# Kernel tuning notes

Hardware: AMD Instinct MI355X
Metric: run time of the kernel (lower is better)

The kernel has to match this reference:

```python
import jax, jax.numpy as jnp
import numpy as np

N_HEADS = 4

def log_cosh(x):
    # numerically stable log(cosh(x)) = |x| + log1p(exp(-2|x|)) - log(2)
    ax = jnp.abs(x)
    return ax + jnp.log1p(jnp.exp(-2.0 * ax)) - jnp.log(2.0)

def setup_inputs() -> dict:
    key = jax.random.key(0)
    ks = jax.random.split(key, 7)
    B, I, A, E, H = 4, 2048, 2048, 256, N_HEADS
    return {
        "query": jax.random.normal(ks[0], (B, I, E), dtype=jnp.float32),
        "key": jax.random.normal(ks[1], (B, A, E), dtype=jnp.float32),
        "value": jax.random.normal(ks[2], (B, A, E), dtype=jnp.float32),
        "distances": jax.random.uniform(ks[3], (B, I, A), dtype=jnp.float32),
        "in_proj_w": jax.random.normal(ks[4], (3 * E, E), dtype=jnp.float32) * 0.05,
        "out_proj_w": jax.random.normal(ks[5], (E, E), dtype=jnp.float32) * 0.05,
        "mass_w": jax.random.normal(ks[6], (H, E), dtype=jnp.float32) * 0.05,
    }

def reference(query, key, value, distances, in_proj_w, out_proj_w, mass_w):
    B, I, E = query.shape
    A = key.shape[1]
    H = N_HEADS
    D = E // H
    # distance-decay additive bias: mass is (B, A, H), nonnegative via log_cosh
    mass = log_cosh(key @ mass_w.T)                       # (B, A, H)
    bias = jnp.einsum('bah,bia->bhia', -mass, distances)  # (B, H, I, A)
    # nn.MultiheadAttention (bias=False) projections
    wq, wk, wv = jnp.split(in_proj_w, 3, axis=0)          # each (E, E)
    q = (query @ wq.T).reshape(B, I, H, D).transpose(0, 2, 1, 3)  # (B,H,I,D)
    k = (key @ wk.T).reshape(B, A, H, D).transpose(0, 2, 1, 3)    # (B,H,A,D)
    v = (value @ wv.T).reshape(B, A, H, D).transpose(0, 2, 1, 3)  # (B,H,A,D)
    scale = 1.0 / jnp.sqrt(jnp.asarray(D, dtype=q.dtype))
    scores = jnp.einsum('bhid,bhad->bhia', q, k) * scale + bias
    attn = jax.nn.softmax(scores, axis=-1)
    o = jnp.einsum('bhia,bhad->bhid', attn, v)            # (B,H,I,D)
    o = o.transpose(0, 2, 1, 3).reshape(B, I, E)
    return o @ out_proj_w.T
```

## Files before the change

### kernel.cpp

```cpp
#include <hip/hip_runtime.h>
#include <hip/hip_bf16.h>
#include <math.h>

#define BB 4
#define II 2048
#define AA 2048
#define EE 256
#define HH 4

#define LOG2E 1.4426950408889634f
#define SCL   (0.125f * LOG2E)

typedef __bf16 bf16_t;
typedef bf16_t bf16x8 __attribute__((ext_vector_type(8)));
typedef bf16_t bf16x4 __attribute__((ext_vector_type(4)));
typedef float  f32x4  __attribute__((ext_vector_type(4)));

static __device__ __forceinline__ f32x4 mfma16(bf16x8 a, bf16x8 b, f32x4 c) {
    return __builtin_amdgcn_mfma_f32_16x16x32_bf16(a, b, c, 0, 0, 0);
}

static __device__ __forceinline__ void glds16(const bf16_t* g, const bf16_t* l) {
    __builtin_amdgcn_global_load_lds(
        (const __attribute__((address_space(1))) void*)g,
        (__attribute__((address_space(3))) void*)l, 16, 0, 0);
}

static __device__ __forceinline__ void proj_body(
    const float* __restrict__ Aop, const float* __restrict__ Bop,
    bf16_t* __restrict__ Cout, int m0, int n0, int TRANS, float cscale,
    bf16_t (*sA)[72], bf16_t (*sB)[72])
{
    const int t = threadIdx.x;
    const int w = t >> 6, l = t & 63, g = l >> 4, q = l & 15;
    const int wm = w >> 1, wn = w & 1;
    const int r = t >> 2, s = t & 3;

    f32x4 acc[2][2] = {};

    for (int kt = 0; kt < 4; ++kt) {
        {
            const float* ga = Aop + (size_t)(m0 + r) * EE + kt * 64 + s * 16;
            float tmp[16];
            *(f32x4*)&tmp[0]  = *(const f32x4*)(ga + 0);
            *(f32x4*)&tmp[4]  = *(const f32x4*)(ga + 4);
            *(f32x4*)&tmp[8]  = *(const f32x4*)(ga + 8);
            *(f32x4*)&tmp[12] = *(const f32x4*)(ga + 12);
            bf16x8 w0, w1;
            #pragma unroll
            for (int i = 0; i < 8; ++i) { w0[i] = (bf16_t)tmp[i]; w1[i] = (bf16_t)tmp[8 + i]; }
            *(bf16x8*)&sA[r][s * 16]     = w0;
            *(bf16x8*)&sA[r][s * 16 + 8] = w1;
        }
        {
            const float* gb = Bop + (size_t)(n0 + r) * EE + kt * 64 + s * 16;
            float tmp[16];
            *(f32x4*)&tmp[0]  = *(const f32x4*)(gb + 0);
            *(f32x4*)&tmp[4]  = *(const f32x4*)(gb + 4);
            *(f32x4*)&tmp[8]  = *(const f32x4*)(gb + 8);
            *(f32x4*)&tmp[12] = *(const f32x4*)(gb + 12);
            bf16x8 w0, w1;
            #pragma unroll
            for (int i = 0; i < 8; ++i) { w0[i] = (bf16_t)tmp[i]; w1[i] = (bf16_t)tmp[8 + i]; }
            *(bf16x8*)&sB[r][s * 16]     = w0;
            *(bf16x8*)&sB[r][s * 16 + 8] = w1;
        }
        __syncthreads();
        #pragma unroll
        for (int ks = 0; ks < 2; ++ks) {
            bf16x8 aA[2], aB[2];
            #pragma unroll
            for (int f = 0; f < 2; ++f) {
                aA[f] = *(const bf16x8*)&sA[wm * 32 + f * 16 + q][ks * 32 + g * 8];
                aB[f] = *(const bf16x8*)&sB[wn * 32 + f * 16 + q][ks * 32 + g * 8];
            }
            #pragma unroll
            for (int fm = 0; fm < 2; ++fm)
            #pragma unroll
            for (int fn = 0; fn < 2; ++fn)
                acc[fm][fn] = mfma16(aA[fm], aB[fn], acc[fm][fn]);
        }
        __syncthreads();
    }
    #pragma unroll
    for (int fm = 0; fm < 2; ++fm)
    #pragma unroll
    for (int fn = 0; fn < 2; ++fn)
    #pragma unroll
    for (int j = 0; j < 4; ++j) {
        const int m = m0 + wm * 32 + fm * 16 + g * 4 + j;
        const int n = n0 + wn * 32 + fn * 16 + q;
        const bf16_t v = (bf16_t)(acc[fm][fn][j] * cscale);
        if (TRANS == 0) {
            Cout[(size_t)m * EE + n] = v;
        } else {
            const int bb = n >> 11, a = n & (AA - 1);
            const int a6 = a & 63;
            const int p6 = (a6 & 32) | ((a6 & 12) << 1) | ((a6 & 16) >> 2) | (a6 & 3);
            Cout[(size_t)bb * (AA * EE) + (size_t)(a >> 6) * (EE * 64) + m * 64 + p6] = v;
        }
    }
}

__global__ __launch_bounds__(256) void fused_pre(
    const float* __restrict__ query, const float* __restrict__ key,
    const float* __restrict__ value, const float* __restrict__ in_w,
    const float* __restrict__ mass_w,
    bf16_t* __restrict__ Qp, bf16_t* __restrict__ Kp, bf16_t* __restrict__ Vt,
    float* __restrict__ massT)
{
    __shared__ __align__(16) bf16_t sA[64][72];
    __shared__ __align__(16) bf16_t sB[64][72];
    const int z = blockIdx.z;
    if (z == 0) {
        proj_body(query, in_w, Qp, blockIdx.x * 64, blockIdx.y * 64, 0, SCL, sA, sB);
    } else if (z == 1) {
        proj_body(key, in_w + 65536, Kp, blockIdx.x * 64, blockIdx.y * 64, 0, 1.0f, sA, sB);
    } else if (z == 2) {
        proj_body(in_w + 131072, value, Vt, blockIdx.y * 64, blockIdx.x * 64, 1, 1.0f, sA, sB);
    } else {
        const int w = threadIdx.x >> 6, l = threadIdx.x & 63;
        const int p = blockIdx.y * 128 + blockIdx.x;
        const int row0 = p * 16 + w * 4;
        f32x4 mw[HH];
        #pragma unroll
        for (int hh = 0; hh < HH; ++hh)
            mw[hh] = *(const f32x4*)(mass_w + hh * EE + l * 4);
        #pragma unroll
        for (int rr = 0; rr < 4; ++rr) {
            const int row = row0 + rr;
            f32x4 kv = *(const f32x4*)(key + (size_t)row * EE + l * 4);
            f32x4 sd;
            #pragma unroll
            for (int hh = 0; hh < HH; ++hh)
                sd[hh] = kv[0]*mw[hh][0] + kv[1]*mw[hh][1] + kv[2]*mw[hh][2] + kv[3]*mw[hh][3];
            #pragma unroll
            for (int off = 32; off >= 1; off >>= 1) {
                #pragma unroll
                for (int hh = 0; hh < HH; ++hh) sd[hh] += __shfl_xor(sd[hh], off, 64);
            }
            if (l == 0) {
                const int bb = row >> 11, a = row & (AA - 1);
                #pragma unroll
                for (int hh = 0; hh < HH; ++hh) {
                    float ax = fabsf(sd[hh]);
                    massT[((size_t)bb * HH + hh) * AA + a] =
                        (ax + log1pf(__expf(-2.0f * ax)) - 0.693147180559945f) * LOG2E;
                }
            }
        }
    }
}

__global__ __launch_bounds__(256) void out_gemm(
    const bf16_t* __restrict__ Aop, const float* __restrict__ Bop,
    float* __restrict__ Cout)
{
    __shared__ __align__(16) bf16_t sA[64][72];
    __shared__ __align__(16) bf16_t sB[64][72];
    const int t = threadIdx.x;
    const int w = t >> 6, l = t & 63, g = l >> 4, q = l & 15;
    const int wm = w >> 1, wn = w & 1;
    const int m0 = blockIdx.x * 64, n0 = blockIdx.y * 64;
    const int r = t >> 2, s = t & 3;

    f32x4 acc[2][2] = {};

    for (int kt = 0; kt < 4; ++kt) {
        {
            const bf16_t* ga = Aop + (size_t)(m0 + r) * EE + kt * 64 + s * 16;
            *(bf16x8*)&sA[r][s * 16]     = *(const bf16x8*)(ga);
            *(bf16x8*)&sA[r][s * 16 + 8] = *(const bf16x8*)(ga + 8);
        }
        {
            const float* gb = Bop + (size_t)(n0 + r) * EE + kt * 64 + s * 16;
            float tmp[16];
            *(f32x4*)&tmp[0]  = *(const f32x4*)(gb + 0);
            *(f32x4*)&tmp[4]  = *(const f32x4*)(gb + 4);
            *(f32x4*)&tmp[8]  = *(const f32x4*)(gb + 8);
            *(f32x4*)&tmp[12] = *(const f32x4*)(gb + 12);
            bf16x8 w0, w1;
            #pragma unroll
            for (int i = 0; i < 8; ++i) { w0[i] = (bf16_t)tmp[i]; w1[i] = (bf16_t)tmp[8 + i]; }
            *(bf16x8*)&sB[r][s * 16]     = w0;
            *(bf16x8*)&sB[r][s * 16 + 8] = w1;
        }
        __syncthreads();
        #pragma unroll
        for (int ks = 0; ks < 2; ++ks) {
            bf16x8 aA[2], aB[2];
            #pragma unroll
            for (int f = 0; f < 2; ++f) {
                aA[f] = *(const bf16x8*)&sA[wm * 32 + f * 16 + q][ks * 32 + g * 8];
                aB[f] = *(const bf16x8*)&sB[wn * 32 + f * 16 + q][ks * 32 + g * 8];
            }
            #pragma unroll
            for (int fm = 0; fm < 2; ++fm)
            #pragma unroll
            for (int fn = 0; fn < 2; ++fn)
                acc[fm][fn] = mfma16(aA[fm], aB[fn], acc[fm][fn]);
        }
        __syncthreads();
    }
    #pragma unroll
    for (int fm = 0; fm < 2; ++fm)
    #pragma unroll
    for (int fn = 0; fn < 2; ++fn)
    #pragma unroll
    for (int j = 0; j < 4; ++j) {
        const int m = m0 + wm * 32 + fm * 16 + g * 4 + j;
        const int n = n0 + wn * 32 + fn * 16 + q;
        Cout[(size_t)m * EE + n] = acc[fm][fn][j];
    }
}

__global__ __launch_bounds__(256, 4) void attn_kernel(
    const bf16_t* __restrict__ Qp, const bf16_t* __restrict__ Kp,
    const bf16_t* __restrict__ Vt, const float* __restrict__ massT,
    const float* __restrict__ dist, bf16_t* __restrict__ Obuf)
{
    __shared__ __align__(16) bf16_t sK[2][4096];
    __shared__ __align__(16) bf16_t sV[2][4096];
    __shared__ __align__(16) float  sM[2048];

    const int t = threadIdx.x;
    const int rg = t >> 6, l = t & 63, g = l >> 4, q = l & 15;
    const int h = blockIdx.y, b = blockIdx.z;
    const int i0 = blockIdx.x * 64;

    *(f32x4*)&sM[t * 8]     = *(const f32x4*)(massT + ((size_t)b * HH + h) * AA + t * 8);
    *(f32x4*)&sM[t * 8 + 4] = *(const f32x4*)(massT + ((size_t)b * HH + h) * AA + t * 8 + 4);

    bf16x8 qf[2];
    #pragma unroll
    for (int ks = 0; ks < 2; ++ks)
        qf[ks] = *(const bf16x8*)(Qp + (size_t)(b * II + i0 + rg * 16 + q) * EE
                                     + h * 64 + ks * 32 + g * 8);

    const int u0 = rg * 2;
    const int drow0 = u0 * 8 + (l >> 3);
    const int cs = (l & 7) ^ (drow0 & 7);

    const bf16_t* pkg = Kp + ((size_t)b * AA + drow0) * EE + h * 64 + cs * 8;
    const bf16_t* pvg = Vt + (size_t)b * (AA * EE) + (size_t)(h * 64 + drow0) * 64 + cs * 8;
    const float*  pdg = dist + ((size_t)b * II + i0 + rg * 16 + q) * AA + g * 4;

    auto stage = [&](int kb) {
        #pragma unroll
        for (int u = 0; u < 2; ++u) {
            glds16(pkg + u * (8 * EE), &sK[kb][(u0 + u) * 512]);
            glds16(pvg + u * (8 * 64), &sV[kb][(u0 + u) * 512]);
        }
    };

    f32x4 rd[2][4];

    stage(0);
    pkg += 64 * EE; pvg += EE * 64;
    #pragma unroll
    for (int fa = 0; fa < 4; ++fa) rd[0][fa] = *(const f32x4*)(pdg + fa * 16);
    pdg += 64;
    __syncthreads();

    float mrun = -INFINITY;
    f32x4 oacc[4] = {};
    f32x4 lacc = {};
    bf16x8 vone;
    #pragma unroll
    for (int j = 0; j < 8; ++j) vone[j] = (bf16_t)1.0f;

    int ma = 0;

    #pragma unroll 2
    for (int k = 0; k < 32; ++k) {
        const int kb = k & 1;
        if (k < 31) {
            stage(kb ^ 1);
            pkg += 64 * EE; pvg += EE * 64;
            #pragma unroll
            for (int fa = 0; fa < 4; ++fa)
                rd[(k + 1) & 1][fa] = *(const f32x4*)(pdg + fa * 16);
            pdg += 64;
        }

        f32x4 st[4] = {};
        __builtin_amdgcn_s_setprio(1);
        #pragma unroll
        for (int fa = 0; fa < 4; ++fa) {
            const int row = fa * 16 + q;
            #pragma unroll
            for (int ks = 0; ks < 2; ++ks) {
                bf16x8 ak = *(const bf16x8*)&sK[kb][row * 64 + (((ks * 4 + g) ^ (row & 7)) * 8)];
                st[fa] = mfma16(ak, qf[ks], st[fa]);
            }
        }
        __builtin_amdgcn_s_setprio(0);

        float mloc = -INFINITY;
        #pragma unroll
        for (int fa = 0; fa < 4; ++fa) {
            f32x4 ms = *(const f32x4*)&sM[ma + fa * 16 + g * 4];
            #pragma unroll
            for (int j = 0; j < 4; ++j) {
                float sv = fmaf(-ms[j], rd[kb][fa][j], st[fa][j]);
                st[fa][j] = sv;
                mloc = fmaxf(mloc, sv);
            }
        }
        ma += 64;

        mloc = fmaxf(mloc, __shfl_xor(mloc, 16, 64));
        mloc = fmaxf(mloc, __shfl_xor(mloc, 32, 64));
        const bool skip = __all(mloc <= mrun + 8.0f);
        float mnew = mrun;
        if (!skip) {
            mnew = fmaxf(mrun, mloc);
            const float sc = exp2f(mrun - mnew);
            mrun = mnew;
            float osc[4];
            #pragma unroll
            for (int j = 0; j < 4; ++j) osc[j] = __shfl(sc, g * 4 + j, 64);
            #pragma unroll
            for (int fd = 0; fd < 4; ++fd)
            #pragma unroll
            for (int j = 0; j < 4; ++j) oacc[fd][j] *= osc[j];
            #pragma unroll
            for (int j = 0; j < 4; ++j) lacc[j] *= osc[j];
        }

        #pragma unroll
        for (int fa = 0; fa < 4; ++fa)
        #pragma unroll
        for (int j = 0; j < 4; ++j)
            st[fa][j] = exp2f(st[fa][j] - mnew);

        bf16x8 pa[2];
        #pragma unroll
        for (int ka = 0; ka < 2; ++ka)
        #pragma unroll
        for (int j = 0; j < 8; ++j)
            pa[ka][j] = (bf16_t)st[2 * ka + (j >> 2)][j & 3];

        __builtin_amdgcn_s_setprio(1);
        #pragma unroll
        for (int ka = 0; ka < 2; ++ka) {
            #pragma unroll
            for (int fd = 0; fd < 4; ++fd) {
                const int row = fd * 16 + q;
                bf16x8 bv = *(const bf16x8*)&sV[kb][row * 64 + (((ka * 4 + g) ^ (row & 7)) * 8)];
                oacc[fd] = mfma16(pa[ka], bv, oacc[fd]);
            }
            lacc = mfma16(pa[ka], vone, lacc);
        }
        __builtin_amdgcn_s_setprio(0);

        __syncthreads();
    }

    f32x4 inv;
    #pragma unroll
    for (int j = 0; j < 4; ++j) inv[j] = 1.0f / lacc[j];
    #pragma unroll
    for (int fd = 0; fd < 4; ++fd)
    #pragma unroll
    for (int j = 0; j < 4; ++j) {
        Obuf[(size_t)(b * II + i0 + rg * 16 + g * 4 + j) * EE
             + h * 64 + fd * 16 + q] = (bf16_t)(oacc[fd][j] * inv[j]);
    }
}

extern "C" void kernel_launch(void* const* d_in, const int* in_sizes, int n_in,
                              void* d_out, int out_size, void* d_ws, size_t ws_size,
                              hipStream_t stream)
{
    const float* query  = (const float*)d_in[0];
    const float* key    = (const float*)d_in[1];
    const float* value  = (const float*)d_in[2];
    const float* dist   = (const float*)d_in[3];
    const float* in_w   = (const float*)d_in[4];
    const float* out_w  = (const float*)d_in[5];
    const float* mass_w = (const float*)d_in[6];
    float* out = (float*)d_out;

    char* ws = (char*)d_ws;
    bf16_t* Qp    = (bf16_t*)(ws);
    bf16_t* Kp    = (bf16_t*)(ws + 1 * 4194304);
    bf16_t* Vt    = (bf16_t*)(ws + 2 * 4194304);
    bf16_t* Obuf  = (bf16_t*)(ws + 3 * 4194304);
    float*  massT = (float*) (ws + 4 * 4194304);

    fused_pre<<<dim3(128, 4, 4), dim3(256), 0, stream>>>(
        query, key, value, in_w, mass_w, Qp, Kp, Vt, massT);
    attn_kernel<<<dim3(32, 4, 4), dim3(256), 0, stream>>>(Qp, Kp, Vt, massT, dist, Obuf);
    out_gemm<<<dim3(128, 4), dim3(256), 0, stream>>>(Obuf, out_w, out);
}
```

Baseline: 86.74 us.

## Split attention over key chunks and drop online-max rescaling

The attention kernel now splits the 2048 keys into four chunks per query tile, giving four times as many blocks. Each block writes unnormalized fp32 partial outputs and row sums to a workspace. The output GEMM adds the four partials, divides by the summed denominators and converts to bf16 before multiplying. The running-max subtraction and rescaling are removed, and mass is read from global memory into registers instead of shared memory. This adds extra global writes and reads for the partials, and without max subtraction exp2 can overflow if scores grow large.

```diff
diff --git a/kernel.cpp b/kernel.cpp
--- a/kernel.cpp
+++ b/kernel.cpp
@@ -152,9 +152,140 @@
     }
 }
 
+__global__ __launch_bounds__(256, 5) void attn_kernel(
+    const bf16_t* __restrict__ Qp, const bf16_t* __restrict__ Kp,
+    const bf16_t* __restrict__ Vt, const float* __restrict__ massT,
+    const float* __restrict__ dist, float* __restrict__ Opart,
+    float* __restrict__ Lpart)
+{
+    __shared__ __align__(16) bf16_t sK[2][4096];
+    __shared__ __align__(16) bf16_t sV[2][4096];
+
+    const int t = threadIdx.x;
+    const int rg = t >> 6, l = t & 63, g = l >> 4, q = l & 15;
+    const int it = blockIdx.x >> 2, qa = blockIdx.x & 3;
+    const int h = blockIdx.y, b = blockIdx.z;
+    const int i0 = it * 64;
+    const int a0 = qa * 512;
+
+    bf16x8 qf[2];
+    #pragma unroll
+    for (int ks = 0; ks < 2; ++ks)
+        qf[ks] = *(const bf16x8*)(Qp + (size_t)(b * II + i0 + rg * 16 + q) * EE
+                                     + h * 64 + ks * 32 + g * 8);
+
+    const int u0 = rg * 2;
+    const int drow0 = u0 * 8 + (l >> 3);
+    const int cs = (l & 7) ^ (drow0 & 7);
+
+    const bf16_t* pkg = Kp + ((size_t)b * AA + a0 + drow0) * EE + h * 64 + cs * 8;
+    const bf16_t* pvg = Vt + (size_t)b * (AA * EE) + (size_t)(a0 >> 6) * (EE * 64)
+                           + (size_t)(h * 64 + drow0) * 64 + cs * 8;
+    const float*  pdg = dist + ((size_t)b * II + i0 + rg * 16 + q) * AA + a0 + g * 4;
+    const float*  pmg = massT + ((size_t)b * HH + h) * AA + a0 + g * 4;
+
+    auto stage = [&](int kb) {
+        #pragma unroll
+        for (int u = 0; u < 2; ++u) {
+            glds16(pkg + u * (8 * EE), &sK[kb][(u0 + u) * 512]);
+            glds16(pvg + u * (8 * 64), &sV[kb][(u0 + u) * 512]);
+        }
+    };
+
+    f32x4 rd[2][4];
+    f32x4 rm[2][4];
+
+    stage(0);
+    pkg += 64 * EE; pvg += EE * 64;
+    #pragma unroll
+    for (int fa = 0; fa < 4; ++fa) {
+        rd[0][fa] = *(const f32x4*)(pdg + fa * 16);
+        rm[0][fa] = *(const f32x4*)(pmg + fa * 16);
+    }
+    pdg += 64; pmg += 64;
+    __syncthreads();
+
+    f32x4 oacc[4] = {};
+    f32x4 lacc = {};
+    bf16x8 vone;
+    #pragma unroll
+    for (int j = 0; j < 8; ++j) vone[j] = (bf16_t)1.0f;
+
+    #pragma unroll 2
+    for (int k = 0; k < 8; ++k) {
+        const int kb = k & 1;
+        if (k < 7) {
+            stage(kb ^ 1);
+            pkg += 64 * EE; pvg += EE * 64;
+            #pragma unroll
+            for (int fa = 0; fa < 4; ++fa) {
+                rd[kb ^ 1][fa] = *(const f32x4*)(pdg + fa * 16);
+                rm[kb ^ 1][fa] = *(const f32x4*)(pmg + fa * 16);
+            }
+            pdg += 64; pmg += 64;
+        }
+
+        f32x4 st[4] = {};
+        __builtin_amdgcn_s_setprio(1);
+        #pragma unroll
+        for (int fa = 0; fa < 4; ++fa) {
+            const int row = fa * 16 + q;
+            #pragma unroll
+            for (int ks = 0; ks < 2; ++ks) {
+                bf16x8 ak = *(const bf16x8*)&sK[kb][row * 64 + (((ks * 4 + g) ^ (row & 7)) * 8)];
+                st[fa] = mfma16(ak, qf[ks], st[fa]);
+            }
+        }
+        __builtin_amdgcn_s_setprio(0);
+
+        #pragma unroll
+        for (int fa = 0; fa < 4; ++fa) {
+            #pragma unroll
+            for (int j = 0; j < 4; ++j)
+                st[fa][j] = exp2f(fmaf(-rm[kb][fa][j], rd[kb][fa][j], st[fa][j]));
+        }
+
+        bf16x8 pa[2];
+        #pragma unroll
+        for (int ka = 0; ka < 2; ++ka)
+        #pragma unroll
+        for (int j = 0; j < 8; ++j)
+            pa[ka][j] = (bf16_t)st[2 * ka + (j >> 2)][j & 3];
+
+        __builtin_amdgcn_s_setprio(1);
+        #pragma unroll
+        for (int ka = 0; ka < 2; ++ka) {
+            #pragma unroll
+            for (int fd = 0; fd < 4; ++fd) {
+                const int row = fd * 16 + q;
+                bf16x8 bv = *(const bf16x8*)&sV[kb][row * 64 + (((ka * 4 + g) ^ (row & 7)) * 8)];
+                oacc[fd] = mfma16(pa[ka], bv, oacc[fd]);
+            }
+            lacc = mfma16(pa[ka], vone, lacc);
+        }
+        __builtin_amdgcn_s_setprio(0);
+
+        __syncthreads();
+    }
+
+    float* Oq = Opart + (size_t)qa * ((size_t)BB * II * EE);
+    #pragma unroll
+    for (int fd = 0; fd < 4; ++fd)
+    #pragma unroll
+    for (int j = 0; j < 4; ++j)
+        Oq[(size_t)(b * II + i0 + rg * 16 + g * 4 + j) * EE + h * 64 + fd * 16 + q]
+            = oacc[fd][j];
+    if (q == 0) {
+        float* Lq = Lpart + (size_t)qa * (BB * HH * II);
+        #pragma unroll
+        for (int j = 0; j < 4; ++j)
+            Lq[((size_t)b * HH + h) * II + i0 + rg * 16 + g * 4 + j] = lacc[j];
+    }
+}
+
 __global__ __launch_bounds__(256) void out_gemm(
-    const bf16_t* __restrict__ Aop, const float* __restrict__ Bop,
-    float* __restrict__ Cout)
+    const float* __restrict__ Opart, const float* __restrict__ Lpart,
+    const float* __restrict__ Bop, float* __restrict__ Cout)
 {
     __shared__ __align__(16) bf16_t sA[64][72];
     __shared__ __align__(16) bf16_t sB[64][72];
@@ -164,13 +295,35 @@
     const int m0 = blockIdx.x * 64, n0 = blockIdx.y * 64;
     const int r = t >> 2, s = t & 3;
 
+    const size_t OQ = (size_t)BB * II * EE;
+    const size_t LQ = (size_t)BB * HH * II;
+
     f32x4 acc[2][2] = {};
 
     for (int kt = 0; kt < 4; ++kt) {
         {
-            const bf16_t* ga = Aop + (size_t)(m0 + r) * EE + kt * 64 + s * 16;
-            *(bf16x8*)&sA[r][s * 16]     = *(const bf16x8*)(ga);
-            *(bf16x8*)&sA[r][s * 16 + 8] = *(const bf16x8*)(ga + 8);
+            const int m = m0 + r;
+            const size_t lidx = ((size_t)(m >> 11) * HH + kt) * II + (m & (II - 1));
+            const float lsum = Lpart[lidx] + Lpart[LQ + lidx]
+                             + Lpart[2 * LQ + lidx] + Lpart[3 * LQ + lidx];
+            const float invl = 1.0f / lsum;
+            const float* po = Opart + (size_t)m * EE + kt * 64 + s * 16;
+            bf16x8 w0, w1;
+            #pragma unroll
+            for (int vv = 0; vv < 4; ++vv) {
+                f32x4 a4 = *(const f32x4*)(po + vv * 4);
+                a4 = a4 + *(const f32x4*)(po + OQ + vv * 4);
+                a4 = a4 + *(const f32x4*)(po + 2 * OQ + vv * 4);
+                a4 = a4 + *(const f32x4*)(po + 3 * OQ + vv * 4);
+                #pragma unroll
+                for (int j = 0; j < 4; ++j) {
+                    const bf16_t v = (bf16_t)(a4[j] * invl);
+                    if (vv < 2) w0[vv * 4 + j] = v;
+                    else        w1[(vv - 2) * 4 + j] = v;
+                }
+            }
+            *(bf16x8*)&sA[r][s * 16]     = w0;
+            *(bf16x8*)&sA[r][s * 16 + 8] = w1;
         }
         {
             const float* gb = Bop + (size_t)(n0 + r) * EE + kt * 64 + s * 16;
@@ -214,161 +367,6 @@
     }
 }
 
-__global__ __launch_bounds__(256, 4) void attn_kernel(
-    const bf16_t* __restrict__ Qp, const bf16_t* __restrict__ Kp,
-    const bf16_t* __restrict__ Vt, const float* __restrict__ massT,
-    const float* __restrict__ dist, bf16_t* __restrict__ Obuf)
-{
-    __shared__ __align__(16) bf16_t sK[2][4096];
-    __shared__ __align__(16) bf16_t sV[2][4096];
-    __shared__ __align__(16) float  sM[2048];
-
-    const int t = threadIdx.x;
-    const int rg = t >> 6, l = t & 63, g = l >> 4, q = l & 15;
-    const int h = blockIdx.y, b = blockIdx.z;
-    const int i0 = blockIdx.x * 64;
-
-    *(f32x4*)&sM[t * 8]     = *(const f32x4*)(massT + ((size_t)b * HH + h) * AA + t * 8);
-    *(f32x4*)&sM[t * 8 + 4] = *(const f32x4*)(massT + ((size_t)b * HH + h) * AA + t * 8 + 4);
-
-    bf16x8 qf[2];
-    #pragma unroll
-    for (int ks = 0; ks < 2; ++ks)
-        qf[ks] = *(const bf16x8*)(Qp + (size_t)(b * II + i0 + rg * 16 + q) * EE
-                                     + h * 64 + ks * 32 + g * 8);
-
-    const int u0 = rg * 2;
-    const int drow0 = u0 * 8 + (l >> 3);
-    const int cs = (l & 7) ^ (drow0 & 7);
-
-    const bf16_t* pkg = Kp + ((size_t)b * AA + drow0) * EE + h * 64 + cs * 8;
-    const bf16_t* pvg = Vt + (size_t)b * (AA * EE) + (size_t)(h * 64 + drow0) * 64 + cs * 8;
-    const float*  pdg = dist + ((size_t)b * II + i0 + rg * 16 + q) * AA + g * 4;
-
-    auto stage = [&](int kb) {
-        #pragma unroll
-        for (int u = 0; u < 2; ++u) {
-            glds16(pkg + u * (8 * EE), &sK[kb][(u0 + u) * 512]);
-            glds16(pvg + u * (8 * 64), &sV[kb][(u0 + u) * 512]);
-        }
-    };
-
-    f32x4 rd[2][4];
-
-    stage(0);
-    pkg += 64 * EE; pvg += EE * 64;
-    #pragma unroll
-    for (int fa = 0; fa < 4; ++fa) rd[0][fa] = *(const f32x4*)(pdg + fa * 16);
-    pdg += 64;
-    __syncthreads();
-
-    float mrun = -INFINITY;
-    f32x4 oacc[4] = {};
-    f32x4 lacc = {};
-    bf16x8 vone;
-    #pragma unroll
-    for (int j = 0; j < 8; ++j) vone[j] = (bf16_t)1.0f;
-
-    int ma = 0;
-
-    #pragma unroll 2
-    for (int k = 0; k < 32; ++k) {
-        const int kb = k & 1;
-        if (k < 31) {
-            stage(kb ^ 1);
-            pkg += 64 * EE; pvg += EE * 64;
-            #pragma unroll
-            for (int fa = 0; fa < 4; ++fa)
-                rd[(k + 1) & 1][fa] = *(const f32x4*)(pdg + fa * 16);
-            pdg += 64;
-        }
-
-        f32x4 st[4] = {};
-        __builtin_amdgcn_s_setprio(1);
-        #pragma unroll
-        for (int fa = 0; fa < 4; ++fa) {
-            const int row = fa * 16 + q;
-            #pragma unroll
-            for (int ks = 0; ks < 2; ++ks) {
-                bf16x8 ak = *(const bf16x8*)&sK[kb][row * 64 + (((ks * 4 + g) ^ (row & 7)) * 8)];
-                st[fa] = mfma16(ak, qf[ks], st[fa]);
-            }
-        }
-        __builtin_amdgcn_s_setprio(0);
-
-        float mloc = -INFINITY;
-        #pragma unroll
-        for (int fa = 0; fa < 4; ++fa) {
-            f32x4 ms = *(const f32x4*)&sM[ma + fa * 16 + g * 4];
-            #pragma unroll
-            for (int j = 0; j < 4; ++j) {
-                float sv = fmaf(-ms[j], rd[kb][fa][j], st[fa][j]);
-                st[fa][j] = sv;
-                mloc = fmaxf(mloc, sv);
-            }
-        }
-        ma += 64;
-
-        mloc = fmaxf(mloc, __shfl_xor(mloc, 16, 64));
-        mloc = fmaxf(mloc, __shfl_xor(mloc, 32, 64));
-        const bool skip = __all(mloc <= mrun + 8.0f);
-        float mnew = mrun;
-        if (!skip) {
-            mnew = fmaxf(mrun, mloc);
-            const float sc = exp2f(mrun - mnew);
-            mrun = mnew;
-            float osc[4];
-            #pragma unroll
-            for (int j = 0; j < 4; ++j) osc[j] = __shfl(sc, g * 4 + j, 64);
-            #pragma unroll
-            for (int fd = 0; fd < 4; ++fd)
-            #pragma unroll
-            for (int j = 0; j < 4; ++j) oacc[fd][j] *= osc[j];
-            #pragma unroll
-            for (int j = 0; j < 4; ++j) lacc[j] *= osc[j];
-        }
-
-        #pragma unroll
-        for (int fa = 0; fa < 4; ++fa)
-        #pragma unroll
-        for (int j = 0; j < 4; ++j)
-            st[fa][j] = exp2f(st[fa][j] - mnew);
-
-        bf16x8 pa[2];
-        #pragma unroll
-        for (int ka = 0; ka < 2; ++ka)
-        #pragma unroll
-        for (int j = 0; j < 8; ++j)
-            pa[ka][j] = (bf16_t)st[2 * ka + (j >> 2)][j & 3];
-
-        __builtin_amdgcn_s_setprio(1);
-        #pragma unroll
-        for (int ka = 0; ka < 2; ++ka) {
-            #pragma unroll
-            for (int fd = 0; fd < 4; ++fd) {
-                const int row = fd * 16 + q;
-                bf16x8 bv = *(const bf16x8*)&sV[kb][row * 64 + (((ka * 4 + g) ^ (row & 7)) * 8)];
-                oacc[fd] = mfma16(pa[ka], bv, oacc[fd]);
-            }
-            lacc = mfma16(pa[ka], vone, lacc);
-        }
-        __builtin_amdgcn_s_setprio(0);
-
-        __syncthreads();
-    }
-
-    f32x4 inv;
-    #pragma unroll
-    for (int j = 0; j < 4; ++j) inv[j] = 1.0f / lacc[j];
-    #pragma unroll
-    for (int fd = 0; fd < 4; ++fd)
-    #pragma unroll
-    for (int j = 0; j < 4; ++j) {
-        Obuf[(size_t)(b * II + i0 + rg * 16 + g * 4 + j) * EE
-             + h * 64 + fd * 16 + q] = (bf16_t)(oacc[fd][j] * inv[j]);
-    }
-}
-
 extern "C" void kernel_launch(void* const* d_in, const int* in_sizes, int n_in,
                               void* d_out, int out_size, void* d_ws, size_t ws_size,
                               hipStream_t stream)
@@ -386,11 +384,13 @@
     bf16_t* Qp    = (bf16_t*)(ws);
     bf16_t* Kp    = (bf16_t*)(ws + 1 * 4194304);
     bf16_t* Vt    = (bf16_t*)(ws + 2 * 4194304);
-    bf16_t* Obuf  = (bf16_t*)(ws + 3 * 4194304);
-    float*  massT = (float*) (ws + 4 * 4194304);
+    float*  massT = (float*) (ws + 3 * 4194304);
+    float*  Opart = (float*) (ws + 4 * 4194304);
+    float*  Lpart = (float*) (ws + 12 * 4194304);
 
     fused_pre<<<dim3(128, 4, 4), dim3(256), 0, stream>>>(
         query, key, value, in_w, mass_w, Qp, Kp, Vt, massT);
-    attn_kernel<<<dim3(32, 4, 4), dim3(256), 0, stream>>>(Qp, Kp, Vt, massT, dist, Obuf);
-    out_gemm<<<dim3(128, 4), dim3(256), 0, stream>>>(Obuf, out_w, out);
-}
+    attn_kernel<<<dim3(128, 4, 4), dim3(256), 0, stream>>>(
+        Qp, Kp, Vt, massT, dist, Opart, Lpart);
+    out_gemm<<<dim3(128, 4), dim3(256), 0, stream>>>(Opart, Lpart, out_w, out);
+}
```

Measured after the change: 260.9 us. 201% more time.
